# Optimization experiments

Hardware: AMD Instinct MI355X
Metric: run time of the kernel (lower is better)

## Reference

```python
import jax, jax.numpy as jnp
import numpy as np

B, N, C, Cn, M = 4, 8192, 128, 64, 32


def _window(x, M):
    # torch F.pad(x, [0,0, M//2, M//2-1]) + unfold(dim=1, size=M, step=1)
    # x: [B, N, Cn] -> [B, N, M, Cn]
    Bx, Nx, Cx = x.shape
    p = M // 2
    xp = jnp.pad(x, ((0, 0), (p, M - 1 - p), (0, 0)))
    idx = jnp.arange(Nx)[:, None] + jnp.arange(M)[None, :]  # [N, M]
    return xp[:, idx, :]  # [B, N, M, Cn]


def setup_inputs() -> dict:
    key = jax.random.key(0)
    ks = jax.random.split(key, 9)
    q = jax.random.normal(ks[0], (B, N, C), dtype=jnp.float32)
    k = jax.random.normal(ks[1], (B, N, C), dtype=jnp.float32)
    v = jax.random.normal(ks[2], (B, N, C), dtype=jnp.float32)
    pe = jax.random.normal(ks[3], (B, N, M, Cn), dtype=jnp.float32)
    # Linear weights stored as [in, out]; scaled like torch default init (~1/sqrt(fan_in)).
    Wq = jax.random.normal(ks[4], (C, Cn), dtype=jnp.float32) / np.sqrt(C)
    Wk = jax.random.normal(ks[5], (C, Cn), dtype=jnp.float32) / np.sqrt(C)
    Wv = jax.random.normal(ks[6], (C, Cn), dtype=jnp.float32) / np.sqrt(C)
    w_sa1 = jax.random.normal(ks[7], (Cn,), dtype=jnp.float32) / np.sqrt(Cn)
    w_sa2 = jax.random.normal(ks[8], (Cn, C), dtype=jnp.float32) / np.sqrt(Cn)
    return {"q": q, "k": k, "v": v, "pe": pe, "Wq": Wq, "Wk": Wk, "Wv": Wv,
            "w_sa1": w_sa1, "w_sa2": w_sa2}


def reference(q, k, v, pe, Wq, Wk, Wv, w_sa1, w_sa2):
    Mw = pe.shape[2]
    qp = q @ Wq  # [B, N, Cn]
    kp = k @ Wk
    vp = v @ Wv
    k_m = _window(kp, Mw)  # [B, N, M, Cn]
    v_m = _window(vp, Mw)  # [B, N, M, Cn]
    # subtraction-based scoring + tiny linear to scalar
    sa = qp[:, :, None, :] - k_m + pe               # [B, N, M, Cn]
    logits = jnp.einsum('bnmc,c->bnm', sa, w_sa1)    # [B, N, M]
    scores = jax.nn.softmax(logits, axis=-1)         # [B, N, M]
    # original: matmul(scores[B,1,N,M], (v_m+pe).permute(0,3,2,1)[B,Cn,M,N]) -> [B,Cn,N,N], sum over last axis.
    # Equivalent: reduce (v_m + pe) over the position axis first, then contract over M.
    S = jnp.sum(v_m + pe, axis=1)                    # [B, M, Cn]
    p_attn = jnp.einsum('bnm,bmc->bnc', scores, S)   # [B, N, Cn]
    out = p_attn @ w_sa2                             # [B, N, C]
    return out  # dropout is identity at eval
```

## Files before the change

kernel.cpp:

```cpp
#include <hip/hip_runtime.h>
#include <math.h>

#define B_ 4
#define N_ 8192
#define C_ 128
#define CN_ 64
#define M_ 32

#define ROR1 0x121
#define ROR2 0x122
#define ROR4 0x124
#define ROR8 0x128

typedef float f4 __attribute__((ext_vector_type(4)));
typedef float f2 __attribute__((ext_vector_type(2)));

__device__ __forceinline__ f4 ld4(const float* p) { return *(const f4*)p; }

template<int CTRL>
__device__ __forceinline__ float dpp_add(float x) {
    int y = __builtin_amdgcn_update_dpp(0, __float_as_int(x), CTRL, 0xF, 0xF, true);
    return x + __int_as_float(y);
}
template<int CTRL>
__device__ __forceinline__ float dpp_max(float x) {
    int y = __builtin_amdgcn_update_dpp(0, __float_as_int(x), CTRL, 0xF, 0xF, true);
    return fmaxf(x, __int_as_float(y));
}
__device__ __forceinline__ float red16_add(float x) {
    return dpp_add<ROR1>(dpp_add<ROR2>(dpp_add<ROR4>(dpp_add<ROR8>(x))));
}
__device__ __forceinline__ float red16_max(float x) {
    return dpp_max<ROR1>(dpp_max<ROR2>(dpp_max<ROR4>(dpp_max<ROR8>(x))));
}

__global__ __launch_bounds__(256) void k1(const float* __restrict__ q,
                                          const float* __restrict__ k,
                                          const float* __restrict__ v,
                                          const float* __restrict__ Wq,
                                          const float* __restrict__ Wk,
                                          const float* __restrict__ w1,
                                          float* __restrict__ vsum_part,
                                          float* __restrict__ a_ws,
                                          float* __restrict__ kb_ws) {
    int g = blockIdx.x;
    int t = threadIdx.x;
    if (g < 256) {
        int b = g >> 6;
        int chunk = g & 63;
        const float* vb = v + ((size_t)b * N_ + (size_t)chunk * 128) * C_;
        int c4 = t & 31, h = t >> 5;
        f4 acc = (f4){0.f, 0.f, 0.f, 0.f};
        for (int r = h; r < 128; r += 8) acc += ld4(vb + (size_t)r * C_ + c4 * 4);
        __shared__ f4 red[256];
        red[t] = acc;
        __syncthreads();
        if (t < 32) {
            f4 s = red[t];
#pragma unroll
            for (int i = 1; i < 8; ++i) s += red[i * 32 + t];
            *((f4*)(vsum_part + (size_t)g * C_) + t) = s;
        }
    } else {
        int gg = g - 256;
        __shared__ float wq1l[C_], wk1l[C_];
        if (t < C_) {
            float s = 0.f;
            for (int c2 = 0; c2 < CN_; ++c2) s += Wq[t * CN_ + c2] * w1[c2];
            wq1l[t] = s;
        } else {
            int c = t - C_;
            float s = 0.f;
            for (int c2 = 0; c2 < CN_; ++c2) s += Wk[c * CN_ + c2] * w1[c2];
            wk1l[c] = s;
        }
        __syncthreads();
        int lane = t & 63, wv = t >> 6;
        int grp = lane >> 4, li = lane & 15;
        f4 wq0 = *((const f4*)wq1l + li * 2);
        f4 wq1v = *((const f4*)wq1l + li * 2 + 1);
        f4 wk0 = *((const f4*)wk1l + li * 2);
        f4 wk1v = *((const f4*)wk1l + li * 2 + 1);
        int r0 = gg * 128 + wv * 32;
        for (int it = 0; it < 8; ++it) {
            int r = r0 + it * 4 + grp;
            const float* qr = q + (size_t)r * C_;
            const float* kr = k + (size_t)r * C_;
            f4 x0 = ld4(qr + li * 8), x1 = ld4(qr + li * 8 + 4);
            f4 y0 = ld4(kr + li * 8), y1 = ld4(kr + li * 8 + 4);
            float ta = x0.x * wq0.x + x0.y * wq0.y + x0.z * wq0.z + x0.w * wq0.w
                     + x1.x * wq1v.x + x1.y * wq1v.y + x1.z * wq1v.z + x1.w * wq1v.w;
            float tk = y0.x * wk0.x + y0.y * wk0.y + y0.z * wk0.z + y0.w * wk0.w
                     + y1.x * wk1v.x + y1.y * wk1v.y + y1.z * wk1v.z + y1.w * wk1v.w;
            ta = red16_add(ta);
            tk = red16_add(tk);
            if (li == 0) { a_ws[r] = ta; kb_ws[r] = tk; }
        }
    }
}

__global__ __launch_bounds__(256) void kPE(const float* __restrict__ pe,
                                           const float* __restrict__ w1,
                                           const float* __restrict__ a_ws,
                                           const float* __restrict__ kb_ws,
                                           float* __restrict__ scl_g,
                                           float* __restrict__ pe_part) {
    int g = blockIdx.x;
    int b = g >> 8;
    int n0 = (g & 255) * 32;
    int t = threadIdx.x;
    int lane = t & 63, wv = t >> 6;
    int grp = lane >> 4, li = lane & 15;
    f4 w1v = *((const f4*)w1 + li);

    __shared__ float lpd[4][256];
    __shared__ f4 lps4[4][256];

    f4 acc[8];
#pragma unroll
    for (int j = 0; j < 8; ++j) acc[j] = (f4){0.f, 0.f, 0.f, 0.f};

    int nbase = n0 + wv * 8;
    const float* pbase = pe + ((size_t)b * N_ + (size_t)nbase) * (size_t)(M_ * CN_);
    for (int i = 0; i < 8; ++i) {
        const float* p = pbase + (size_t)i * (M_ * CN_);
        f4 x[8];
#pragma unroll
        for (int j = 0; j < 8; ++j) x[j] = ld4(p + (j * 64 + lane) * 4);
#pragma unroll
        for (int j = 0; j < 8; ++j) {
            acc[j] += x[j];
            float tv = x[j].x * w1v.x + x[j].y * w1v.y + x[j].z * w1v.z + x[j].w * w1v.w;
            tv = red16_add(tv);
            if (li == 0) lpd[wv][i * 32 + j * 4 + grp] = tv;
        }
    }
    {
        int hw = lane >> 5, m = lane & 31;
        const float* kbb = kb_ws + (size_t)b * N_;
        float* sout = scl_g + ((size_t)b * N_ + (size_t)nbase) * M_;
#pragma unroll
        for (int ii = 0; ii < 4; ++ii) {
            int rl = ii * 2 + hw;
            int n = nbase + rl;
            float pd = lpd[wv][rl * 32 + m];
            int j = n + m - 16;
            float kbm = (j >= 0 && j < N_) ? kbb[j] : 0.f;
            float lg = a_ws[(size_t)b * N_ + n] + pd - kbm;
            float mx = red16_max(lg);
            mx = fmaxf(mx, __shfl_xor(mx, 16));
            float e = __expf(lg - mx);
            float sm = red16_add(e);
            sm += __shfl_xor(sm, 16);
            sout[ii * 64 + lane] = e / sm;
        }
    }
    f4* ppg = (f4*)(pe_part + (size_t)g * (M_ * CN_));
#pragma unroll
    for (int r = 0; r < 2; ++r) {
        __syncthreads();
#pragma unroll
        for (int jr = 0; jr < 4; ++jr) lps4[wv][jr * 64 + lane] = acc[r * 4 + jr];
        __syncthreads();
        f4 s = lps4[0][t];
        s += lps4[1][t];
        s += lps4[2][t];
        s += lps4[3][t];
        ppg[r * 256 + t] = s;
    }
}

__global__ __launch_bounds__(256) void kR(const float* __restrict__ pe_part,
                                          const float* __restrict__ vsum_part,
                                          float* __restrict__ S_sum,
                                          float* __restrict__ vsum_final) {
    int g = blockIdx.x;
    int t = threadIdx.x;
    if (g < 256) {
        int b = g >> 6, ch = g & 63;
        int pg = t >> 5, fi = t & 31;
        const float* base = pe_part + (size_t)b * 256 * 2048 + ch * 32 + fi;
        float a0 = 0.f, a1 = 0.f, a2 = 0.f, a3 = 0.f;
#pragma unroll
        for (int p = pg; p < 256; p += 32) {
            a0 += base[(size_t)p * 2048];
            a1 += base[(size_t)(p + 8) * 2048];
            a2 += base[(size_t)(p + 16) * 2048];
            a3 += base[(size_t)(p + 24) * 2048];
        }
        __shared__ float red[8][32];
        red[pg][fi] = (a0 + a1) + (a2 + a3);
        __syncthreads();
        if (t < 32) {
            float s = red[0][t];
#pragma unroll
            for (int i = 1; i < 8; ++i) s += red[i][t];
            S_sum[(size_t)b * 2048 + ch * 32 + t] = s;
        }
    } else {
        int b = g - 256;
        if (t < C_) {
            const float* vp = vsum_part + (size_t)b * 64 * C_ + t;
            float a0 = 0.f, a1 = 0.f, a2 = 0.f, a3 = 0.f;
#pragma unroll
            for (int i = 0; i < 64; i += 4) {
                a0 += vp[(i + 0) * C_];
                a1 += vp[(i + 1) * C_];
                a2 += vp[(i + 2) * C_];
                a3 += vp[(i + 3) * C_];
            }
            vsum_final[b * C_ + t] = (a0 + a1) + (a2 + a3);
        }
    }
}

__global__ __launch_bounds__(256) void kB2(const float* __restrict__ v,
                                           const float* __restrict__ Wv,
                                           const float* __restrict__ vsum_final,
                                           const float* __restrict__ S_sum,
                                           const float* __restrict__ w2,
                                           float* __restrict__ SW2) {
    int b = blockIdx.x >> 3, seg = blockIdx.x & 7;
    int t = threadIdx.x;
    __shared__ float vd[4][C_];
    __shared__ float Sl[4][CN_];
#pragma unroll
    for (int mlp = 0; mlp < 2; ++mlp) {
        int ml = (t >> 7) + mlp * 2;
        int c = t & 127;
        int m = seg * 4 + ml;
        float excl = 0.f;
        if (m > 16) {
            for (int r = 0; r < m - 16; ++r) excl += v[((size_t)b * N_ + r) * C_ + c];
        } else if (m < 16) {
            for (int r = N_ - (16 - m); r < N_; ++r) excl += v[((size_t)b * N_ + r) * C_ + c];
        }
        vd[ml][c] = vsum_final[b * C_ + c] - excl;
    }
    __syncthreads();
    {
        int ml = t >> 6, c2 = t & 63;
        float s = 0.f;
        for (int c = 0; c < C_; ++c) s += vd[ml][c] * Wv[c * CN_ + c2];
        s += S_sum[(size_t)b * 2048 + (seg * 4 + ml) * CN_ + c2];
        Sl[ml][c2] = s;
    }
    __syncthreads();
#pragma unroll
    for (int pass = 0; pass < 2; ++pass) {
        int ml = (t >> 7) + pass * 2;
        int cc = t & 127;
        float s = 0.f;
#pragma unroll
        for (int c2 = 0; c2 < CN_; ++c2) s += Sl[ml][c2] * w2[c2 * C_ + cc];
        SW2[((size_t)b * M_ + seg * 4 + ml) * C_ + cc] = s;
    }
}

__global__ __launch_bounds__(256) void kOut2(const float* __restrict__ scl_g,
                                             const float* __restrict__ SW2,
                                             float* __restrict__ out) {
    int g = blockIdx.x;
    int b = g >> 7;
    int n0 = (g & 127) * 64;
    int t = threadIdx.x;
    int lane = t & 63, wv = t >> 6;
    __shared__ float scl[64][M_];

    {
        const f4* src = (const f4*)(scl_g + ((size_t)b * N_ + (size_t)n0) * M_);
        f4* dst = (f4*)&scl[0][0];
        dst[t] = src[t];
        dst[256 + t] = src[256 + t];
    }
    f2 sw2[M_];
    {
        const f2* sw2g = (const f2*)(SW2 + (size_t)b * M_ * C_);
#pragma unroll
        for (int mm = 0; mm < M_; ++mm) sw2[mm] = sw2g[mm * 64 + lane];
    }
    __syncthreads();
    for (int i = 0; i < 16; ++i) {
        int r = wv * 16 + i;
        const f4* sp = (const f4*)(&scl[r][0]);
        float ox = 0.f, oy = 0.f;
#pragma unroll
        for (int j4 = 0; j4 < 8; ++j4) {
            f4 s4 = sp[j4];
            ox += s4.x * sw2[j4 * 4 + 0].x; oy += s4.x * sw2[j4 * 4 + 0].y;
            ox += s4.y * sw2[j4 * 4 + 1].x; oy += s4.y * sw2[j4 * 4 + 1].y;
            ox += s4.z * sw2[j4 * 4 + 2].x; oy += s4.z * sw2[j4 * 4 + 2].y;
            ox += s4.w * sw2[j4 * 4 + 3].x; oy += s4.w * sw2[j4 * 4 + 3].y;
        }
        size_t u = (size_t)b * N_ + (size_t)(n0 + r);
        f2 o; o.x = ox; o.y = oy;
        *((f2*)(out + u * C_) + lane) = o;
    }
}

extern "C" void kernel_launch(void* const* d_in, const int* in_sizes, int n_in,
                              void* d_out, int out_size, void* d_ws, size_t ws_size,
                              hipStream_t stream) {
    const float* q  = (const float*)d_in[0];
    const float* k  = (const float*)d_in[1];
    const float* v  = (const float*)d_in[2];
    const float* pe = (const float*)d_in[3];
    const float* Wq = (const float*)d_in[4];
    const float* Wk = (const float*)d_in[5];
    const float* Wv = (const float*)d_in[6];
    const float* w1 = (const float*)d_in[7];
    const float* w2 = (const float*)d_in[8];
    float* out = (float*)d_out;
    float* ws  = (float*)d_ws;

    float* vsum_part  = ws;
    float* vsum_final = vsum_part + 32768;
    float* a_ws       = vsum_final + 512;
    float* kb_ws      = a_ws + 32768;
    float* scl_g      = kb_ws + 32768;
    float* pe_part    = scl_g + 1048576;
    float* S_sum      = pe_part + 2097152;
    float* SW2        = S_sum + 8192;

    k1   <<<512, 256, 0, stream>>>(q, k, v, Wq, Wk, w1, vsum_part, a_ws, kb_ws);
    kPE  <<<1024, 256, 0, stream>>>(pe, w1, a_ws, kb_ws, scl_g, pe_part);
    kR   <<<260, 256, 0, stream>>>(pe_part, vsum_part, S_sum, vsum_final);
    kB2  <<<32, 256, 0, stream>>>(v, Wv, vsum_final, S_sum, w2, SW2);
    kOut2<<<512, 256, 0, stream>>>(scl_g, SW2, out);
}
```

Baseline: 98.71 us.

## Double-buffer pe loads through LDS with async global_load_lds in kPE

The kPE kernel's direct global loads of the pe tensor are replaced by per-wave double-buffered asynchronous global-to-LDS copies. Each wave issues the next half-row into LDS, waits on vmcnt, then reads the current half with inline ds_read_b128. This is meant to overlap the memory traffic of the dominant pe stream with the reduction and dot-product work. The final cross-wave reduction now reuses the same LDS buffer and drops one sync round. In exchange the kernel uses more LDS, which may lower occupancy, and it relies on hand-written waitcnt assembly.

```diff
diff --git a/kernel.cpp b/kernel.cpp
--- a/kernel.cpp
+++ b/kernel.cpp
@@ -32,6 +32,12 @@
 }
 __device__ __forceinline__ float red16_max(float x) {
     return dpp_max<ROR1>(dpp_max<ROR2>(dpp_max<ROR4>(dpp_max<ROR8>(x))));
+}
+
+__device__ __forceinline__ void cp16(float* lds, const float* g) {
+    __builtin_amdgcn_global_load_lds(
+        (const __attribute__((address_space(1))) void*)g,
+        (__attribute__((address_space(3))) void*)lds, 16, 0, 0);
 }
 
 __global__ __launch_bounds__(256) void k1(const float* __restrict__ q,
@@ -99,6 +105,34 @@
     }
 }
 
+#define CONS(xv, jg, iv) \
+    { acc[jg] += xv; \
+      float tv = xv.x * w1v.x + xv.y * w1v.y + xv.z * w1v.z + xv.w * w1v.w; \
+      tv = red16_add(tv); \
+      if (li == 0) lpd[wv][(iv) * 32 + (jg) * 4 + grp] = tv; }
+
+#define STEP(H) { \
+    if ((H) < 15) { \
+        const float* rp = pbase + (size_t)(((H) + 1) >> 1) * 2048 + (((H) + 1) & 1) * 1024 + lane * 4; \
+        float* ld = bufw + (((H) + 1) & 1) * 1024; \
+        cp16(ld, rp); cp16(ld + 256, rp + 256); cp16(ld + 512, rp + 512); cp16(ld + 768, rp + 768); \
+        asm volatile("s_waitcnt vmcnt(4)" ::: "memory"); \
+    } else { \
+        asm volatile("s_waitcnt vmcnt(0)" ::: "memory"); \
+    } \
+    f4 x0, x1, x2, x3; \
+    { uint32_t a = lbase + ((H) & 1) * 4096 + lane * 16; \
+      asm volatile("ds_read_b128 %0, %4 offset:0\n\t" \
+                   "ds_read_b128 %1, %4 offset:1024\n\t" \
+                   "ds_read_b128 %2, %4 offset:2048\n\t" \
+                   "ds_read_b128 %3, %4 offset:3072\n\t" \
+                   "s_waitcnt lgkmcnt(0)" \
+                   : "=v"(x0), "=v"(x1), "=v"(x2), "=v"(x3) : "v"(a) : "memory"); } \
+    CONS(x0, ((H) & 1) * 4 + 0, (H) >> 1) \
+    CONS(x1, ((H) & 1) * 4 + 1, (H) >> 1) \
+    CONS(x2, ((H) & 1) * 4 + 2, (H) >> 1) \
+    CONS(x3, ((H) & 1) * 4 + 3, (H) >> 1) }
+
 __global__ __launch_bounds__(256) void kPE(const float* __restrict__ pe,
                                            const float* __restrict__ w1,
                                            const float* __restrict__ a_ws,
@@ -114,27 +148,27 @@
     f4 w1v = *((const f4*)w1 + li);
 
     __shared__ float lpd[4][256];
-    __shared__ f4 lps4[4][256];
+    __shared__ __align__(16) float buf[8192];
 
     f4 acc[8];
 #pragma unroll
     for (int j = 0; j < 8; ++j) acc[j] = (f4){0.f, 0.f, 0.f, 0.f};
 
     int nbase = n0 + wv * 8;
-    const float* pbase = pe + ((size_t)b * N_ + (size_t)nbase) * (size_t)(M_ * CN_);
-    for (int i = 0; i < 8; ++i) {
-        const float* p = pbase + (size_t)i * (M_ * CN_);
-        f4 x[8];
-#pragma unroll
-        for (int j = 0; j < 8; ++j) x[j] = ld4(p + (j * 64 + lane) * 4);
-#pragma unroll
-        for (int j = 0; j < 8; ++j) {
-            acc[j] += x[j];
-            float tv = x[j].x * w1v.x + x[j].y * w1v.y + x[j].z * w1v.z + x[j].w * w1v.w;
-            tv = red16_add(tv);
-            if (li == 0) lpd[wv][i * 32 + j * 4 + grp] = tv;
-        }
-    }
+    const float* pbase = pe + ((size_t)b * N_ + (size_t)nbase) * 2048;
+    float* bufw = &buf[wv * 2048];
+    uint32_t lbase = (uint32_t)(uintptr_t)(__attribute__((address_space(3))) float*)bufw;
+
+    {
+        const float* rp = pbase + lane * 4;
+        cp16(bufw, rp); cp16(bufw + 256, rp + 256);
+        cp16(bufw + 512, rp + 512); cp16(bufw + 768, rp + 768);
+    }
+    STEP(0)  STEP(1)  STEP(2)  STEP(3)
+    STEP(4)  STEP(5)  STEP(6)  STEP(7)
+    STEP(8)  STEP(9)  STEP(10) STEP(11)
+    STEP(12) STEP(13) STEP(14) STEP(15)
+
     {
         int hw = lane >> 5, m = lane & 31;
         const float* kbb = kb_ws + (size_t)b * N_;
@@ -155,18 +189,17 @@
             sout[ii * 64 + lane] = e / sm;
         }
     }
-    f4* ppg = (f4*)(pe_part + (size_t)g * (M_ * CN_));
-#pragma unroll
-    for (int r = 0; r < 2; ++r) {
-        __syncthreads();
-#pragma unroll
-        for (int jr = 0; jr < 4; ++jr) lps4[wv][jr * 64 + lane] = acc[r * 4 + jr];
-        __syncthreads();
-        f4 s = lps4[0][t];
-        s += lps4[1][t];
-        s += lps4[2][t];
-        s += lps4[3][t];
-        ppg[r * 256 + t] = s;
+    __syncthreads();
+    f4* lps = (f4*)buf;
+#pragma unroll
+    for (int j = 0; j < 8; ++j) lps[wv * 512 + j * 64 + lane] = acc[j];
+    __syncthreads();
+    f4* ppg = (f4*)(pe_part + (size_t)g * 2048);
+#pragma unroll
+    for (int i2 = 0; i2 < 2; ++i2) {
+        int idx = i2 * 256 + t;
+        f4 s = lps[idx] + lps[512 + idx] + lps[1024 + idx] + lps[1536 + idx];
+        ppg[idx] = s;
     }
 }
 
```

After: 101.5 us. 2.9% more time.

## Fuse q/k projection and v-sum kernel into PE scoring kernel

Applied to the files above, without the earlier changes.

Merges the first kernel (v column sums plus q·(Wq w1) and k·(Wk w1) projections) into the pe scoring kernel as one launch. Each pe block now computes its own 32 query projections and 64 windowed key projections (with a halo) into shared memory, and extra blocks handle the v sums. This removes one launch and the global round trip through a_ws/kb_ws. In exchange, every block recomputes Wq·w1 and Wk·w1, and the k rows are read twice because the halos overlap.

```diff
diff --git a/kernel.cpp b/kernel.cpp
--- a/kernel.cpp
+++ b/kernel.cpp
@@ -34,36 +34,33 @@
     return dpp_max<ROR1>(dpp_max<ROR2>(dpp_max<ROR4>(dpp_max<ROR8>(x))));
 }
 
-__global__ __launch_bounds__(256) void k1(const float* __restrict__ q,
+__global__ __launch_bounds__(256) void kA(const float* __restrict__ q,
                                           const float* __restrict__ k,
                                           const float* __restrict__ v,
+                                          const float* __restrict__ pe,
                                           const float* __restrict__ Wq,
                                           const float* __restrict__ Wk,
                                           const float* __restrict__ w1,
                                           float* __restrict__ vsum_part,
-                                          float* __restrict__ a_ws,
-                                          float* __restrict__ kb_ws) {
+                                          float* __restrict__ scl_g,
+                                          float* __restrict__ pe_part) {
+    __shared__ float lpd[4][256];
+    __shared__ __align__(16) f4 lps4[4][256];
+    __shared__ float pro[352];
+
     int g = blockIdx.x;
     int t = threadIdx.x;
-    if (g < 256) {
-        int b = g >> 6;
-        int chunk = g & 63;
-        const float* vb = v + ((size_t)b * N_ + (size_t)chunk * 128) * C_;
-        int c4 = t & 31, h = t >> 5;
-        f4 acc = (f4){0.f, 0.f, 0.f, 0.f};
-        for (int r = h; r < 128; r += 8) acc += ld4(vb + (size_t)r * C_ + c4 * 4);
-        __shared__ f4 red[256];
-        red[t] = acc;
-        __syncthreads();
-        if (t < 32) {
-            f4 s = red[t];
-#pragma unroll
-            for (int i = 1; i < 8; ++i) s += red[i * 32 + t];
-            *((f4*)(vsum_part + (size_t)g * C_) + t) = s;
-        }
-    } else {
-        int gg = g - 256;
-        __shared__ float wq1l[C_], wk1l[C_];
+    int lane = t & 63, wv = t >> 6;
+
+    if (g < 1024) {
+        int b = g >> 8;
+        int n0 = (g & 255) * 32;
+        int grp = lane >> 4, li = lane & 15;
+        float* wq1l = pro;
+        float* wk1l = pro + 128;
+        float* aL   = pro + 256;
+        float* kbL  = pro + 288;
+
         if (t < C_) {
             float s = 0.f;
             for (int c2 = 0; c2 < CN_; ++c2) s += Wq[t * CN_ + c2] * w1[c2];
@@ -75,98 +72,108 @@
             wk1l[c] = s;
         }
         __syncthreads();
-        int lane = t & 63, wv = t >> 6;
-        int grp = lane >> 4, li = lane & 15;
-        f4 wq0 = *((const f4*)wq1l + li * 2);
-        f4 wq1v = *((const f4*)wq1l + li * 2 + 1);
-        f4 wk0 = *((const f4*)wk1l + li * 2);
-        f4 wk1v = *((const f4*)wk1l + li * 2 + 1);
-        int r0 = gg * 128 + wv * 32;
-        for (int it = 0; it < 8; ++it) {
-            int r = r0 + it * 4 + grp;
-            const float* qr = q + (size_t)r * C_;
-            const float* kr = k + (size_t)r * C_;
-            f4 x0 = ld4(qr + li * 8), x1 = ld4(qr + li * 8 + 4);
-            f4 y0 = ld4(kr + li * 8), y1 = ld4(kr + li * 8 + 4);
-            float ta = x0.x * wq0.x + x0.y * wq0.y + x0.z * wq0.z + x0.w * wq0.w
-                     + x1.x * wq1v.x + x1.y * wq1v.y + x1.z * wq1v.z + x1.w * wq1v.w;
-            float tk = y0.x * wk0.x + y0.y * wk0.y + y0.z * wk0.z + y0.w * wk0.w
-                     + y1.x * wk1v.x + y1.y * wk1v.y + y1.z * wk1v.z + y1.w * wk1v.w;
-            ta = red16_add(ta);
-            tk = red16_add(tk);
-            if (li == 0) { a_ws[r] = ta; kb_ws[r] = tk; }
-        }
-    }
-}
-
-__global__ __launch_bounds__(256) void kPE(const float* __restrict__ pe,
-                                           const float* __restrict__ w1,
-                                           const float* __restrict__ a_ws,
-                                           const float* __restrict__ kb_ws,
-                                           float* __restrict__ scl_g,
-                                           float* __restrict__ pe_part) {
-    int g = blockIdx.x;
-    int b = g >> 8;
-    int n0 = (g & 255) * 32;
-    int t = threadIdx.x;
-    int lane = t & 63, wv = t >> 6;
-    int grp = lane >> 4, li = lane & 15;
-    f4 w1v = *((const f4*)w1 + li);
-
-    __shared__ float lpd[4][256];
-    __shared__ f4 lps4[4][256];
-
-    f4 acc[8];
-#pragma unroll
-    for (int j = 0; j < 8; ++j) acc[j] = (f4){0.f, 0.f, 0.f, 0.f};
-
-    int nbase = n0 + wv * 8;
-    const float* pbase = pe + ((size_t)b * N_ + (size_t)nbase) * (size_t)(M_ * CN_);
-    for (int i = 0; i < 8; ++i) {
-        const float* p = pbase + (size_t)i * (M_ * CN_);
-        f4 x[8];
-#pragma unroll
-        for (int j = 0; j < 8; ++j) x[j] = ld4(p + (j * 64 + lane) * 4);
-#pragma unroll
-        for (int j = 0; j < 8; ++j) {
-            acc[j] += x[j];
-            float tv = x[j].x * w1v.x + x[j].y * w1v.y + x[j].z * w1v.z + x[j].w * w1v.w;
-            tv = red16_add(tv);
-            if (li == 0) lpd[wv][i * 32 + j * 4 + grp] = tv;
-        }
-    }
-    {
-        int hw = lane >> 5, m = lane & 31;
-        const float* kbb = kb_ws + (size_t)b * N_;
-        float* sout = scl_g + ((size_t)b * N_ + (size_t)nbase) * M_;
-#pragma unroll
-        for (int ii = 0; ii < 4; ++ii) {
-            int rl = ii * 2 + hw;
-            int n = nbase + rl;
-            float pd = lpd[wv][rl * 32 + m];
-            int j = n + m - 16;
-            float kbm = (j >= 0 && j < N_) ? kbb[j] : 0.f;
-            float lg = a_ws[(size_t)b * N_ + n] + pd - kbm;
-            float mx = red16_max(lg);
-            mx = fmaxf(mx, __shfl_xor(mx, 16));
-            float e = __expf(lg - mx);
-            float sm = red16_add(e);
-            sm += __shfl_xor(sm, 16);
-            sout[ii * 64 + lane] = e / sm;
-        }
-    }
-    f4* ppg = (f4*)(pe_part + (size_t)g * (M_ * CN_));
-#pragma unroll
-    for (int r = 0; r < 2; ++r) {
+
+        {
+            f4 wk0 = *((const f4*)wk1l + li * 2);
+            f4 wk1v = *((const f4*)wk1l + li * 2 + 1);
+#pragma unroll
+            for (int it = 0; it < 4; ++it) {
+                int rl = wv * 16 + it * 4 + grp;
+                int jrow = n0 - 16 + rl;
+                float tk = 0.f;
+                if (jrow >= 0 && jrow < N_) {
+                    const float* kr = k + ((size_t)b * N_ + jrow) * C_;
+                    f4 y0 = ld4(kr + li * 8), y1 = ld4(kr + li * 8 + 4);
+                    tk = y0.x * wk0.x + y0.y * wk0.y + y0.z * wk0.z + y0.w * wk0.w
+                       + y1.x * wk1v.x + y1.y * wk1v.y + y1.z * wk1v.z + y1.w * wk1v.w;
+                }
+                tk = red16_add(tk);
+                if (li == 0) kbL[rl] = tk;
+            }
+            f4 wq0 = *((const f4*)wq1l + li * 2);
+            f4 wq1v = *((const f4*)wq1l + li * 2 + 1);
+#pragma unroll
+            for (int it = 0; it < 2; ++it) {
+                int rl = wv * 8 + it * 4 + grp;
+                const float* qr = q + ((size_t)b * N_ + n0 + rl) * C_;
+                f4 x0 = ld4(qr + li * 8), x1 = ld4(qr + li * 8 + 4);
+                float ta = x0.x * wq0.x + x0.y * wq0.y + x0.z * wq0.z + x0.w * wq0.w
+                         + x1.x * wq1v.x + x1.y * wq1v.y + x1.z * wq1v.z + x1.w * wq1v.w;
+                ta = red16_add(ta);
+                if (li == 0) aL[rl] = ta;
+            }
+        }
         __syncthreads();
-#pragma unroll
-        for (int jr = 0; jr < 4; ++jr) lps4[wv][jr * 64 + lane] = acc[r * 4 + jr];
+
+        f4 w1v = *((const f4*)w1 + li);
+        f4 acc[8];
+#pragma unroll
+        for (int j = 0; j < 8; ++j) acc[j] = (f4){0.f, 0.f, 0.f, 0.f};
+
+        int nbase = n0 + wv * 8;
+        const float* pbase = pe + ((size_t)b * N_ + (size_t)nbase) * 2048;
+        for (int i = 0; i < 8; ++i) {
+            const float* p = pbase + (size_t)i * 2048;
+            f4 x[8];
+#pragma unroll
+            for (int j = 0; j < 8; ++j) x[j] = ld4(p + (j * 64 + lane) * 4);
+#pragma unroll
+            for (int j = 0; j < 8; ++j) {
+                acc[j] += x[j];
+                float tv = x[j].x * w1v.x + x[j].y * w1v.y + x[j].z * w1v.z + x[j].w * w1v.w;
+                tv = red16_add(tv);
+                if (li == 0) lpd[wv][i * 32 + j * 4 + grp] = tv;
+            }
+        }
+
+        {
+            int hw = lane >> 5, m = lane & 31;
+            float* sout = scl_g + ((size_t)b * N_ + (size_t)nbase) * M_;
+#pragma unroll
+            for (int ii = 0; ii < 4; ++ii) {
+                int rl = ii * 2 + hw;
+                int rb = wv * 8 + rl;
+                float pd = lpd[wv][rl * 32 + m];
+                float lg = aL[rb] + pd - kbL[rb + m];
+                float mx = red16_max(lg);
+                mx = fmaxf(mx, __shfl_xor(mx, 16));
+                float e = __expf(lg - mx);
+                float sm = red16_add(e);
+                sm += __shfl_xor(sm, 16);
+                sout[ii * 64 + lane] = e / sm;
+            }
+        }
+
+        f4* ppg = (f4*)(pe_part + (size_t)g * 2048);
+#pragma unroll
+        for (int r = 0; r < 2; ++r) {
+            __syncthreads();
+#pragma unroll
+            for (int jr = 0; jr < 4; ++jr) lps4[wv][jr * 64 + lane] = acc[r * 4 + jr];
+            __syncthreads();
+            f4 s = lps4[0][t];
+            s += lps4[1][t];
+            s += lps4[2][t];
+            s += lps4[3][t];
+            ppg[r * 256 + t] = s;
+        }
+    } else {
+        int gg = g - 1024;
+        int b = gg >> 6;
+        int chunk = gg & 63;
+        const float* vb = v + ((size_t)b * N_ + (size_t)chunk * 128) * C_;
+        int c4 = t & 31, h = t >> 5;
+        f4 acc = (f4){0.f, 0.f, 0.f, 0.f};
+        for (int r = h; r < 128; r += 8) acc += ld4(vb + (size_t)r * C_ + c4 * 4);
+        f4* red = &lps4[0][0];
+        red[t] = acc;
         __syncthreads();
-        f4 s = lps4[0][t];
-        s += lps4[1][t];
-        s += lps4[2][t];
-        s += lps4[3][t];
-        ppg[r * 256 + t] = s;
+        if (t < 32) {
+            f4 s = red[t];
+#pragma unroll
+            for (int i = 1; i < 8; ++i) s += red[i * 32 + t];
+            *((f4*)(vsum_part + (size_t)gg * C_) + t) = s;
+        }
     }
 }
 
@@ -315,15 +322,12 @@
 
     float* vsum_part  = ws;
     float* vsum_final = vsum_part + 32768;
-    float* a_ws       = vsum_final + 512;
-    float* kb_ws      = a_ws + 32768;
-    float* scl_g      = kb_ws + 32768;
+    float* scl_g      = vsum_final + 512;
     float* pe_part    = scl_g + 1048576;
     float* S_sum      = pe_part + 2097152;
     float* SW2        = S_sum + 8192;
 
-    k1   <<<512, 256, 0, stream>>>(q, k, v, Wq, Wk, w1, vsum_part, a_ws, kb_ws);
-    kPE  <<<1024, 256, 0, stream>>>(pe, w1, a_ws, kb_ws, scl_g, pe_part);
+    kA   <<<1280, 256, 0, stream>>>(q, k, v, pe, Wq, Wk, w1, vsum_part, scl_g, pe_part);
     kR   <<<260, 256, 0, stream>>>(pe_part, vsum_part, S_sum, vsum_final);
     kB2  <<<32, 256, 0, stream>>>(v, Wv, vsum_final, S_sum, w2, SW2);
     kOut2<<<512, 256, 0, stream>>>(scl_g, SW2, out);
```

New measurement: 99.86 us. About the same (+1.2%).
